# Kernel tuning notes

Hardware: AMD Instinct MI355X
Metric: run time of the kernel (lower is better)

## Reference

```python
import jax, jax.numpy as jnp
import numpy as np

N_NODES = 100000
N_EDGES = 1600000
IN_FEATS, N_HIDDEN, N_CLASSES = 128, 128, 40


def _sage_layer(h, src, dst, W_self, W_neigh, b):
    # DGL SAGEConv (mean): fc_self(h) + fc_neigh(mean_{u in N_in(v)} h_u)
    msg = h[src]  # [E, F] gather of source-node features
    summed = jax.ops.segment_sum(msg, dst, num_segments=N_NODES)  # [N, F]
    deg = jax.ops.segment_sum(jnp.ones((src.shape[0], 1), h.dtype), dst,
                              num_segments=N_NODES)  # [N, 1] in-degree
    h_neigh = summed / jnp.maximum(deg, 1.0)
    return h @ W_self + b + h_neigh @ W_neigh


def setup_inputs() -> dict:
    key = jax.random.key(0)
    ks = jax.random.split(key, 12)
    inputs = jax.random.normal(ks[0], (N_NODES, IN_FEATS), dtype=jnp.float32)
    src = jax.random.randint(ks[1], (N_EDGES,), 0, N_NODES, dtype=jnp.int64)
    dst = jax.random.randint(ks[2], (N_EDGES,), 0, N_NODES, dtype=jnp.int64)

    def lin(k, fi, fo):
        return jax.random.normal(k, (fi, fo), dtype=jnp.float32) / np.sqrt(fi)

    return {
        "inputs": inputs, "src": src, "dst": dst,
        "W_self0": lin(ks[3], IN_FEATS, N_HIDDEN),
        "W_neigh0": lin(ks[4], IN_FEATS, N_HIDDEN),
        "b0": jnp.zeros((N_HIDDEN,), jnp.float32),
        "W_self1": lin(ks[5], N_HIDDEN, N_HIDDEN),
        "W_neigh1": lin(ks[6], N_HIDDEN, N_HIDDEN),
        "b1": jnp.zeros((N_HIDDEN,), jnp.float32),
        "W_self2": lin(ks[7], N_HIDDEN, N_CLASSES),
        "W_neigh2": lin(ks[8], N_HIDDEN, N_CLASSES),
        "b2": jnp.zeros((N_CLASSES,), jnp.float32),
    }


def reference(inputs, src, dst, W_self0, W_neigh0, b0, W_self1, W_neigh1, b1,
              W_self2, W_neigh2, b2):
    # dropout p=0.0 -> identity
    h = _sage_layer(inputs, src, dst, W_self0, W_neigh0, b0)
    h = jax.nn.relu(h)
    h = _sage_layer(h, src, dst, W_self1, W_neigh1, b1)
    h = jax.nn.relu(h)
    h = _sage_layer(h, src, dst, W_self2, W_neigh2, b2)
    return h
```

## Files before the change

kernel.cpp:

```cpp
#include <hip/hip_runtime.h>


#define F_IN 128

__global__ __launch_bounds__(256) void count_deg_kernel(
    const int* __restrict__ dst, int* __restrict__ cnt, int E) {
    int i = blockIdx.x * 256 + threadIdx.x;
    if (i < E) atomicAdd(&cnt[dst[i]], 1);
}

__global__ __launch_bounds__(1024) void scan_kernel(
    const int* __restrict__ cnt, int* __restrict__ row_ptr, int n) {
    __shared__ int partial[1024];
    int t = threadIdx.x;
    int CH = (n + 1023) >> 10;
    int base = t * CH;
    int s = 0;
    for (int i = 0; i < CH; ++i) {
        int idx = base + i;
        if (idx < n) s += cnt[idx];
    }
    partial[t] = s;
    __syncthreads();
    for (int off = 1; off < 1024; off <<= 1) {
        int v = partial[t];
        int add = (t >= off) ? partial[t - off] : 0;
        __syncthreads();
        partial[t] = v + add;
        __syncthreads();
    }
    int run = (t == 0) ? 0 : partial[t - 1];
    for (int i = 0; i < CH; ++i) {
        int idx = base + i;
        if (idx < n) { row_ptr[idx] = run; run += cnt[idx]; }
    }
    if (t == 1023) row_ptr[n] = run;
}

__global__ __launch_bounds__(256) void fill_kernel(
    const int* __restrict__ src, const int* __restrict__ dst,
    const int* __restrict__ row_ptr, int* __restrict__ cursor,
    int* __restrict__ col, int E) {
    int i = blockIdx.x * 256 + threadIdx.x;
    if (i < E) {
        int d = dst[i];
        int pos = atomicAdd(&cursor[d], 1);
        col[row_ptr[d] + pos] = src[i];
    }
}

__global__ __launch_bounds__(256) void aggregate_kernel(
    const float* __restrict__ h, const int* __restrict__ row_ptr,
    const int* __restrict__ col, float* __restrict__ hn, int n) {
    int g = (blockIdx.x * 256 + threadIdx.x) >> 5;
    int lane = threadIdx.x & 31;
    if (g >= n) return;
    int s = row_ptr[g], e = row_ptr[g + 1];
    const float4* h4 = (const float4*)h;
    float4 acc = make_float4(0.f, 0.f, 0.f, 0.f);
    int i = s;
    for (; i + 3 < e; i += 4) {
        int u0 = col[i], u1 = col[i + 1], u2 = col[i + 2], u3 = col[i + 3];
        float4 x0 = h4[(size_t)u0 * 32 + lane];
        float4 x1 = h4[(size_t)u1 * 32 + lane];
        float4 x2 = h4[(size_t)u2 * 32 + lane];
        float4 x3 = h4[(size_t)u3 * 32 + lane];
        acc.x += (x0.x + x1.x) + (x2.x + x3.x);
        acc.y += (x0.y + x1.y) + (x2.y + x3.y);
        acc.z += (x0.z + x1.z) + (x2.z + x3.z);
        acc.w += (x0.w + x1.w) + (x2.w + x3.w);
    }
    for (; i < e; ++i) {
        int u = col[i];
        float4 x = h4[(size_t)u * 32 + lane];
        acc.x += x.x; acc.y += x.y; acc.z += x.z; acc.w += x.w;
    }
    float inv = 1.f / fmaxf((float)(e - s), 1.f);
    float4 r = make_float4(acc.x * inv, acc.y * inv, acc.z * inv, acc.w * inv);
    ((float4*)hn)[(size_t)g * 32 + lane] = r;
}

template <int NTX, int RPT, int FO_PAD, bool RELU>
__global__ __launch_bounds__(256) void gemm_kernel(
    const float* __restrict__ A, const float* __restrict__ An,
    const float* __restrict__ Ws, const float* __restrict__ Wn,
    const float* __restrict__ b, float* __restrict__ out,
    int n, int fo_real) {
    constexpr int NTY = 256 / NTX;
    __shared__ float As[32][256];
    __shared__ float Wt[32][FO_PAD];

    int t = threadIdx.x;
    int block_row = blockIdx.x * 32;

    #pragma unroll
    for (int j = 0; j < 8; ++j) {
        int f = t + j * 256;
        int r = f >> 6, q = f & 63;
        int node = block_row + r;
        float4 v = make_float4(0.f, 0.f, 0.f, 0.f);
        if (node < n) {
            v = (q < 32) ? ((const float4*)A)[(size_t)node * 32 + q]
                         : ((const float4*)An)[(size_t)node * 32 + (q - 32)];
        }
        ((float4*)&As[r][0])[q] = v;
    }

    float acc[RPT][4];
    #pragma unroll
    for (int i = 0; i < RPT; ++i)
        for (int j = 0; j < 4; ++j) acc[i][j] = 0.f;

    int tx = t % NTX, ty = t / NTX;
    const int c0 = tx * 4;

    for (int kt = 0; kt < 8; ++kt) {
        __syncthreads();
        constexpr int F4 = (32 * FO_PAD / 4) / 256;
        #pragma unroll
        for (int j = 0; j < F4; ++j) {
            int f = t + j * 256;
            int kk = f / (FO_PAD / 4);
            int c4 = f % (FO_PAD / 4);
            int k = kt * 32 + kk;
            const float* Wrow = (k < 128) ? &Ws[(size_t)k * fo_real]
                                          : &Wn[(size_t)(k - 128) * fo_real];
            float4 v;
            if (fo_real == FO_PAD) {
                v = ((const float4*)Wrow)[c4];
            } else {
                int c = c4 * 4;
                v.x = (c + 0 < fo_real) ? Wrow[c + 0] : 0.f;
                v.y = (c + 1 < fo_real) ? Wrow[c + 1] : 0.f;
                v.z = (c + 2 < fo_real) ? Wrow[c + 2] : 0.f;
                v.w = (c + 3 < fo_real) ? Wrow[c + 3] : 0.f;
            }
            ((float4*)&Wt[kk][0])[c4] = v;
        }
        __syncthreads();

        #pragma unroll
        for (int kk = 0; kk < 32; kk += 4) {
            float4 a[RPT];
            #pragma unroll
            for (int i = 0; i < RPT; ++i)
                a[i] = *(const float4*)&As[ty * RPT + i][kt * 32 + kk];
            #pragma unroll
            for (int u = 0; u < 4; ++u) {
                float4 w = ((const float4*)&Wt[kk + u][0])[tx];
                #pragma unroll
                for (int i = 0; i < RPT; ++i) {
                    float av = (&a[i].x)[u];
                    acc[i][0] += av * w.x;
                    acc[i][1] += av * w.y;
                    acc[i][2] += av * w.z;
                    acc[i][3] += av * w.w;
                }
            }
        }
    }

    #pragma unroll
    for (int i = 0; i < RPT; ++i) {
        int node = block_row + ty * RPT + i;
        if (node >= n) continue;
        float4 v;
        v.x = acc[i][0] + b[c0 + 0 < fo_real ? c0 + 0 : 0];
        if (c0 + 4 <= fo_real) {
            v.x = acc[i][0] + b[c0 + 0];
            v.y = acc[i][1] + b[c0 + 1];
            v.z = acc[i][2] + b[c0 + 2];
            v.w = acc[i][3] + b[c0 + 3];
            if (RELU) {
                v.x = fmaxf(v.x, 0.f); v.y = fmaxf(v.y, 0.f);
                v.z = fmaxf(v.z, 0.f); v.w = fmaxf(v.w, 0.f);
            }
            *(float4*)&out[(size_t)node * fo_real + c0] = v;
        } else {
            #pragma unroll
            for (int j = 0; j < 4; ++j) {
                int c = c0 + j;
                if (c < fo_real) {
                    float s = acc[i][j] + b[c];
                    if (RELU) s = fmaxf(s, 0.f);
                    out[(size_t)node * fo_real + c] = s;
                }
            }
        }
    }
}

static inline size_t align256(size_t x) { return (x + 255) & ~(size_t)255; }

extern "C" void kernel_launch(void* const* d_in, const int* in_sizes, int n_in,
                              void* d_out, int out_size, void* d_ws, size_t ws_size,
                              hipStream_t stream) {
    const float* inputs = (const float*)d_in[0];
    const int* src = (const int*)d_in[1];
    const int* dst = (const int*)d_in[2];
    const float* Ws0 = (const float*)d_in[3];
    const float* Wn0 = (const float*)d_in[4];
    const float* b0  = (const float*)d_in[5];
    const float* Ws1 = (const float*)d_in[6];
    const float* Wn1 = (const float*)d_in[7];
    const float* b1  = (const float*)d_in[8];
    const float* Ws2 = (const float*)d_in[9];
    const float* Wn2 = (const float*)d_in[10];
    const float* b2  = (const float*)d_in[11];

    const int N = in_sizes[0] / F_IN;
    const int E = in_sizes[1];

    char* ws = (char*)d_ws;
    size_t off = 0;
    size_t off_cnt    = off; off += align256((size_t)N * 4);
    size_t off_cursor = off; off += align256((size_t)N * 4);
    size_t zero_bytes = off;
    size_t off_rowptr = off; off += align256(((size_t)N + 1) * 4);
    size_t off_col    = off; off += align256((size_t)E * 4);
    size_t off_hneigh = off; off += align256((size_t)N * F_IN * 4);
    size_t off_bufA   = off; off += align256((size_t)N * F_IN * 4);
    size_t off_bufB   = off; off += align256((size_t)N * F_IN * 4);
    (void)ws_size;

    int*   cnt    = (int*)(ws + off_cnt);
    int*   cursor = (int*)(ws + off_cursor);
    int*   rowptr = (int*)(ws + off_rowptr);
    int*   col    = (int*)(ws + off_col);
    float* hneigh = (float*)(ws + off_hneigh);
    float* bufA   = (float*)(ws + off_bufA);
    float* bufB   = (float*)(ws + off_bufB);
    float* out    = (float*)d_out;

    hipMemsetAsync(ws, 0, zero_bytes, stream);

    int eb = (E + 255) / 256;
    count_deg_kernel<<<eb, 256, 0, stream>>>(dst, cnt, E);
    scan_kernel<<<1, 1024, 0, stream>>>(cnt, rowptr, N);
    fill_kernel<<<eb, 256, 0, stream>>>(src, dst, rowptr, cursor, col, E);

    int ab = (N * 32 + 255) / 256;
    int gb = (N + 31) / 32;

    aggregate_kernel<<<ab, 256, 0, stream>>>(inputs, rowptr, col, hneigh, N);
    gemm_kernel<32, 4, 128, true><<<gb, 256, 0, stream>>>(
        inputs, hneigh, Ws0, Wn0, b0, bufA, N, 128);

    aggregate_kernel<<<ab, 256, 0, stream>>>(bufA, rowptr, col, hneigh, N);
    gemm_kernel<32, 4, 128, true><<<gb, 256, 0, stream>>>(
        bufA, hneigh, Ws1, Wn1, b1, bufB, N, 128);

    aggregate_kernel<<<ab, 256, 0, stream>>>(bufB, rowptr, col, hneigh, N);
    gemm_kernel<16, 2, 64, false><<<gb, 256, 0, stream>>>(
        bufB, hneigh, Ws2, Wn2, b2, out, N, 40);
}
```

Before: 1.102 ms.

## Replace single-block prefix scan with three-pass multi-block scan

The single 1024-thread block scan over node degrees is replaced by a three-kernel scan: per-chunk block sums, a scan over those sums, then a per-chunk local scan that adds the block offset. This spreads the scan across many CUs instead of one, where the old version had each thread walk about 98 elements serially with uncoalesced strided access. It adds two extra kernel launches and a small workspace buffer, and it assumes at most 256 chunks (about 262K nodes). The GEMM epilogue also drops a redundant bias read.

Result: faster. 923.1 us (-16.2%).

```diff
diff --git a/kernel.cpp b/kernel.cpp
--- a/kernel.cpp
+++ b/kernel.cpp
@@ -2,6 +2,7 @@
 
 
 #define F_IN 128
+#define SCAN_CHUNK 1024
 
 __global__ __launch_bounds__(256) void count_deg_kernel(
     const int* __restrict__ dst, int* __restrict__ cnt, int E) {
@@ -9,32 +10,69 @@
     if (i < E) atomicAdd(&cnt[dst[i]], 1);
 }
 
-__global__ __launch_bounds__(1024) void scan_kernel(
-    const int* __restrict__ cnt, int* __restrict__ row_ptr, int n) {
-    __shared__ int partial[1024];
+__global__ __launch_bounds__(256) void scan_part1(
+    const int* __restrict__ cnt, int* __restrict__ bsum, int n) {
+    __shared__ int red[4];
+    int base = blockIdx.x * SCAN_CHUNK + threadIdx.x * 4;
+    int s = 0;
+    if (base + 4 <= n) {
+        int4 v = *(const int4*)&cnt[base];
+        s = v.x + v.y + v.z + v.w;
+    } else {
+        for (int j = 0; j < 4; ++j) if (base + j < n) s += cnt[base + j];
+    }
+    for (int off = 32; off > 0; off >>= 1) s += __shfl_down(s, off, 64);
+    if ((threadIdx.x & 63) == 0) red[threadIdx.x >> 6] = s;
+    __syncthreads();
+    if (threadIdx.x == 0)
+        bsum[blockIdx.x] = red[0] + red[1] + red[2] + red[3];
+}
+
+__global__ __launch_bounds__(256) void scan_part2(int* __restrict__ bsum, int nb) {
+    __shared__ int tmp[256];
     int t = threadIdx.x;
-    int CH = (n + 1023) >> 10;
-    int base = t * CH;
+    tmp[t] = (t < nb) ? bsum[t] : 0;
+    __syncthreads();
+    for (int off = 1; off < 256; off <<= 1) {
+        int x = tmp[t];
+        int add = (t >= off) ? tmp[t - off] : 0;
+        __syncthreads();
+        tmp[t] = x + add;
+        __syncthreads();
+    }
+    if (t < nb) bsum[t] = (t == 0) ? 0 : tmp[t - 1];
+}
+
+__global__ __launch_bounds__(256) void scan_part3(
+    const int* __restrict__ cnt, const int* __restrict__ bsum,
+    int* __restrict__ row_ptr, int n, int E) {
+    __shared__ int tsum[256];
+    int t = threadIdx.x;
+    int base = blockIdx.x * SCAN_CHUNK + t * 4;
+    int c[4];
     int s = 0;
-    for (int i = 0; i < CH; ++i) {
-        int idx = base + i;
-        if (idx < n) s += cnt[idx];
-    }
-    partial[t] = s;
+    #pragma unroll
+    for (int j = 0; j < 4; ++j) {
+        int idx = base + j;
+        c[j] = (idx < n) ? cnt[idx] : 0;
+        s += c[j];
+    }
+    tsum[t] = s;
     __syncthreads();
-    for (int off = 1; off < 1024; off <<= 1) {
-        int v = partial[t];
-        int add = (t >= off) ? partial[t - off] : 0;
-        __syncthreads();
-        partial[t] = v + add;
-        __syncthreads();
-    }
-    int run = (t == 0) ? 0 : partial[t - 1];
-    for (int i = 0; i < CH; ++i) {
-        int idx = base + i;
-        if (idx < n) { row_ptr[idx] = run; run += cnt[idx]; }
-    }
-    if (t == 1023) row_ptr[n] = run;
+    for (int off = 1; off < 256; off <<= 1) {
+        int x = tsum[t];
+        int add = (t >= off) ? tsum[t - off] : 0;
+        __syncthreads();
+        tsum[t] = x + add;
+        __syncthreads();
+    }
+    int p = bsum[blockIdx.x] + ((t == 0) ? 0 : tsum[t - 1]);
+    #pragma unroll
+    for (int j = 0; j < 4; ++j) {
+        int idx = base + j;
+        if (idx < n) { row_ptr[idx] = p; p += c[j]; }
+    }
+    if (blockIdx.x == 0 && t == 0) row_ptr[n] = E;
 }
 
 __global__ __launch_bounds__(256) void fill_kernel(
@@ -164,9 +202,8 @@
     for (int i = 0; i < RPT; ++i) {
         int node = block_row + ty * RPT + i;
         if (node >= n) continue;
-        float4 v;
-        v.x = acc[i][0] + b[c0 + 0 < fo_real ? c0 + 0 : 0];
         if (c0 + 4 <= fo_real) {
+            float4 v;
             v.x = acc[i][0] + b[c0 + 0];
             v.y = acc[i][1] + b[c0 + 1];
             v.z = acc[i][2] + b[c0 + 2];
@@ -217,6 +254,7 @@
     size_t off_cursor = off; off += align256((size_t)N * 4);
     size_t zero_bytes = off;
     size_t off_rowptr = off; off += align256(((size_t)N + 1) * 4);
+    size_t off_bsum   = off; off += align256(1024 * 4);
     size_t off_col    = off; off += align256((size_t)E * 4);
     size_t off_hneigh = off; off += align256((size_t)N * F_IN * 4);
     size_t off_bufA   = off; off += align256((size_t)N * F_IN * 4);
@@ -226,6 +264,7 @@
     int*   cnt    = (int*)(ws + off_cnt);
     int*   cursor = (int*)(ws + off_cursor);
     int*   rowptr = (int*)(ws + off_rowptr);
+    int*   bsum   = (int*)(ws + off_bsum);
     int*   col    = (int*)(ws + off_col);
     float* hneigh = (float*)(ws + off_hneigh);
     float* bufA   = (float*)(ws + off_bufA);
@@ -235,8 +274,12 @@
     hipMemsetAsync(ws, 0, zero_bytes, stream);
 
     int eb = (E + 255) / 256;
+    int nb = (N + SCAN_CHUNK - 1) / SCAN_CHUNK;
+
     count_deg_kernel<<<eb, 256, 0, stream>>>(dst, cnt, E);
-    scan_kernel<<<1, 1024, 0, stream>>>(cnt, rowptr, N);
+    scan_part1<<<nb, 256, 0, stream>>>(cnt, bsum, N);
+    scan_part2<<<1, 256, 0, stream>>>(bsum, nb);
+    scan_part3<<<nb, 256, 0, stream>>>(cnt, bsum, rowptr, N, E);
     fill_kernel<<<eb, 256, 0, stream>>>(src, dst, rowptr, cursor, col, E);
 
     int ab = (N * 32 + 255) / 256;
```
